# Kernel optimization log

Measured on AMD Instinct MI355X. Metric: run time of the kernel, lower is better.

The kernel has to match this reference:

```python
import jax, jax.numpy as jnp
import numpy as np

N, E = 50000, 800000
DIM_IN, DIM_H, DIM_OUT, HEADS = 128, 32, 16, 4
HID = DIM_H * HEADS  # 128
FINAL = DIM_OUT * HEADS  # 64
NEG_SLOPE = 0.2


def _glorot(key, shape):
    fan_in, fan_out = shape[0], shape[-1] if len(shape) > 1 else shape[0]
    lim = jnp.sqrt(6.0 / (fan_in + fan_out)).astype(jnp.float32)
    return jax.random.uniform(key, shape, jnp.float32, -lim, lim)


def setup_inputs() -> dict:
    key = jax.random.key(0)
    ks = jax.random.split(key, 16)
    x = jax.random.normal(ks[0], (N, DIM_IN), jnp.float32)
    edge_index = jax.random.randint(ks[1], (2, E), 0, N, dtype=jnp.int64)
    inp = {"x": x, "edge_index": edge_index}
    # layer 1: DIM_IN -> HEADS*DIM_H
    inp["Wl1"] = _glorot(ks[2], (DIM_IN, HEADS * DIM_H))
    inp["Wr1"] = _glorot(ks[3], (DIM_IN, HEADS * DIM_H))
    inp["att1"] = _glorot(ks[4], (HEADS, DIM_H))
    inp["b1"] = jnp.zeros((HEADS * DIM_H,), jnp.float32)
    # layer 2: HID -> HEADS*DIM_H
    inp["Wl2"] = _glorot(ks[5], (HID, HEADS * DIM_H))
    inp["Wr2"] = _glorot(ks[6], (HID, HEADS * DIM_H))
    inp["att2"] = _glorot(ks[7], (HEADS, DIM_H))
    inp["b2"] = jnp.zeros((HEADS * DIM_H,), jnp.float32)
    # layer 3: HID -> HEADS*DIM_OUT
    inp["Wl3"] = _glorot(ks[8], (HID, HEADS * DIM_OUT))
    inp["Wr3"] = _glorot(ks[9], (HID, HEADS * DIM_OUT))
    inp["att3"] = _glorot(ks[10], (HEADS, DIM_OUT))
    inp["b3"] = jnp.zeros((HEADS * DIM_OUT,), jnp.float32)
    return inp


def gatv2_conv(x, src, dst, Wl, Wr, att, b, heads, ch):
    n = x.shape[0]
    xl = (x @ Wl).reshape(n, heads, ch)  # source-side transform
    xr = (x @ Wr).reshape(n, heads, ch)  # target-side transform
    m = xl[src] + xr[dst]                 # [E, H, C]
    e = jnp.einsum('ehc,hc->eh', jax.nn.leaky_relu(m, NEG_SLOPE), att)
    # segment softmax over incoming edges of each dst node
    emax = jax.ops.segment_max(e, dst, num_segments=n)
    ex = jnp.exp(e - emax[dst])
    denom = jax.ops.segment_sum(ex, dst, num_segments=n)
    alpha = ex / denom[dst]               # [E, H]
    out = jax.ops.segment_sum(alpha[:, :, None] * xl[src], dst, num_segments=n)
    return out.reshape(n, heads * ch) + b


def reference(x, edge_index, Wl1, Wr1, att1, b1, Wl2, Wr2, att2, b2, Wl3, Wr3, att3, b3):
    n = x.shape[0]
    loops = jnp.arange(n, dtype=edge_index.dtype)
    src = jnp.concatenate([edge_index[0], loops])  # PyG add_self_loops=True
    dst = jnp.concatenate([edge_index[1], loops])
    # dropout is identity in eval mode
    h = jax.nn.elu(gatv2_conv(x, src, dst, Wl1, Wr1, att1, b1, HEADS, DIM_H))
    h = jax.nn.elu(gatv2_conv(h, src, dst, Wl2, Wr2, att2, b2, HEADS, DIM_H))
    h = gatv2_conv(h, src, dst, Wl3, Wr3, att3, b3, HEADS, DIM_OUT)
    return jax.nn.log_softmax(h, axis=1)
```

## Files before the change

kernel.cpp:

```cpp
#include <hip/hip_runtime.h>
#include <math.h>

constexpr int DIN  = 128;
constexpr int FSH  = 8;
constexpr int NFBM = 200;
constexpr int LCAP = 72;
constexpr int RND  = 4096;
constexpr int FCAP = 4608;

typedef __attribute__((ext_vector_type(8))) short short8;
typedef __attribute__((ext_vector_type(4))) float f32x4;

__device__ __forceinline__ unsigned short f2bf(float f) {
  unsigned u = __float_as_uint(f);
  u = (u + 0x7FFF + ((u >> 16) & 1)) >> 16;
  return (unsigned short)u;
}
__device__ __forceinline__ float bflo(unsigned u) { return __uint_as_float(u << 16); }
__device__ __forceinline__ float bfhi(unsigned u) { return __uint_as_float(u & 0xFFFF0000u); }

__device__ __forceinline__ void unpack8(uint4 u, float* x) {
  x[0] = bflo(u.x); x[1] = bfhi(u.x); x[2] = bflo(u.y); x[3] = bfhi(u.y);
  x[4] = bflo(u.z); x[5] = bfhi(u.z); x[6] = bflo(u.w); x[7] = bfhi(u.w);
}
__device__ __forceinline__ void unpack4(uint2 u, float* x) {
  x[0] = bflo(u.x); x[1] = bfhi(u.x); x[2] = bflo(u.y); x[3] = bfhi(u.y);
}

typedef const __attribute__((address_space(1))) unsigned int guint_t;
typedef __attribute__((address_space(3))) unsigned int luint_t;
__device__ __forceinline__ void async16(const void* g, void* l) {
  __builtin_amdgcn_global_load_lds((guint_t*)g, (luint_t*)l, 16, 0, 0);
}


__global__ __launch_bounds__(256) void prep_kernel(const int* __restrict__ ei,
    int* __restrict__ gcnt, unsigned* __restrict__ gpairs, int E, int nfb, int appb,
    const float* __restrict__ Wl1, const float* __restrict__ Wr1,
    const float* __restrict__ Wl2, const float* __restrict__ Wr2,
    const float* __restrict__ Wl3, const float* __restrict__ Wr3,
    unsigned short* __restrict__ Wt) {
  __shared__ unsigned buf[NFBM * LCAP];
  __shared__ int cnt[NFBM];
  __shared__ int gbase[NFBM];
  const int tid = threadIdx.x;

  if (blockIdx.x >= appb) {
    int e = (blockIdx.x - appb) * 256 + tid;
    if (e >= 81920) return;
    const float* src; int N; int off;
    if (e < 65536) {
      int m = e >> 14; off = e & 16383; N = 128;
      src = (m == 0) ? Wl1 : (m == 1) ? Wr1 : (m == 2) ? Wl2 : Wr2;
    } else {
      int e2 = e - 65536; int m = e2 >> 13; off = e2 & 8191; N = 64;
      src = m ? Wr3 : Wl3;
    }
    int nn = off >> 7, k = off & 127;
    Wt[e] = f2bf(src[(size_t)k * N + nn]);
    return;
  }

  if (tid < NFBM) cnt[tid] = 0;
  __syncthreads();

  const int k0 = blockIdx.x * RND;
  for (int i = tid; i < RND; i += 256) {
    int k = k0 + i;
    if (k >= E) break;
    int src = ei[k], dst = ei[E + k];
    int fb = dst >> FSH;
    int pos = atomicAdd(&cnt[fb], 1);
    if (pos < LCAP)
      buf[fb * LCAP + pos] = (unsigned)src | ((unsigned)(dst & ((1 << FSH) - 1)) << 16);
  }
  __syncthreads();

  if (tid < nfb) gbase[tid] = atomicAdd(&gcnt[tid], min(cnt[tid], LCAP));
  __syncthreads();

  const int wid = tid >> 6, lane = tid & 63;
  for (int fb = wid; fb < nfb; fb += 4) {
    int c  = min(cnt[fb], LCAP);
    int gb = gbase[fb];
    if (gb >= FCAP) continue;
    c = min(c, FCAP - gb);
    unsigned* dstp = gpairs + (size_t)fb * FCAP + gb;
    const unsigned* srcp = &buf[fb * LCAP];
    for (int i = lane; i < c; i += 64) dstp[i] = srcp[i];
  }
}


struct BuildSmem { int hist[1 << FSH]; int wsum[4]; int base_s; };

__device__ __forceinline__ void build_body(BuildSmem& s, int b,
    const unsigned* __restrict__ gpairs, const int* __restrict__ gcnt,
    int* __restrict__ row_ptr, unsigned short* __restrict__ edge_src,
    int n, int nfb) {
  const int tid = threadIdx.x;
  const int lane = tid & 63, wid = tid >> 6;

  const int d0 = b << FSH;
  const int nvalid = min(1 << FSH, n - d0);

  if (wid == 0) {
    int term = 0;
    for (int i = lane; i < b; i += 64)
      term += min(gcnt[i], FCAP) + min(1 << FSH, n - (i << FSH));
#pragma unroll
    for (int o = 32; o >= 1; o >>= 1) term += __shfl_xor(term, o, 64);
    if (lane == 0) s.base_s = term;
  }
  s.hist[tid] = (tid < nvalid) ? 1 : 0;
  __syncthreads();

  const int cnt = min(gcnt[b], FCAP);
  const unsigned* bp = gpairs + (size_t)b * FCAP;
  for (int i = tid; i < cnt; i += 256)
    atomicAdd(&s.hist[bp[i] >> 16], 1);
  __syncthreads();

  const int h = s.hist[tid];
  int incl = h;
#pragma unroll
  for (int o = 1; o < 64; o <<= 1) {
    int t = __shfl_up(incl, o, 64);
    if (lane >= o) incl += t;
  }
  if (lane == 63) s.wsum[wid] = incl;
  __syncthreads();
  int wo = 0;
  for (int wq = 0; wq < wid; ++wq) wo += s.wsum[wq];
  const int base = s.base_s;
  const int excl = wo + incl - h;
  if (tid < nvalid) {
    row_ptr[d0 + tid] = base + excl;
    edge_src[base + excl] = (unsigned short)(d0 + tid);
    s.hist[tid] = excl + 1;
  } else if (d0 + tid == n) {
    row_ptr[n] = base + excl;
  }
  if (b == nfb - 1 && d0 + (1 << FSH) <= n && tid == 0)
    row_ptr[n] = base + cnt + nvalid;
  __syncthreads();

  for (int i = tid; i < cnt; i += 256) {
    unsigned p = bp[i];
    int pos = atomicAdd(&s.hist[p >> 16], 1);
    edge_src[base + pos] = (unsigned short)(p & 0xFFFFu);
  }
}


template<int NC, bool CVT>
__device__ __forceinline__ void gemm2_body(char* lds, int bid, const void* __restrict__ Ap,
    const unsigned short* __restrict__ Wlt, const unsigned short* __restrict__ Wrt,
    unsigned short* __restrict__ outl, unsigned short* __restrict__ outr, int M) {
  constexpr int WNB = NC / 16;
  char* As = lds;
  char* Ws = lds + 16384;
  const int tid  = threadIdx.x;
  const int w    = tid >> 6, lane = tid & 63;
  const int q    = lane >> 4, r15 = lane & 15;
  const int row0 = bid * 64;

  if constexpr (CVT) {
    const float* Af = (const float*)Ap;
    for (int idx = tid * 4; idx < 64 * 128; idx += 1024) {
      int rl = idx >> 7, k = idx & 127;
      int rg = row0 + rl; if (rg >= M) rg = M - 1;
      float4 v = *(const float4*)&Af[(size_t)rg * 128 + k];
      uint2 pk;
      pk.x = (unsigned)f2bf(v.x) | ((unsigned)f2bf(v.y) << 16);
      pk.y = (unsigned)f2bf(v.z) | ((unsigned)f2bf(v.w) << 16);
      char* addr = As + (rl >> 4) * 4096 + (k >> 5) * 1024 +
                   ((((k >> 3) & 3) * 16) + (rl & 15)) * 16 + (k & 7) * 2;
      *(uint2*)addr = pk;
    }
  } else {
    const unsigned short* A = (const unsigned short*)Ap;
    int r = row0 + w * 16 + r15; if (r >= M) r = M - 1;
    const char* g = (const char*)A + (size_t)r * 256 + q * 16;
    char* l = As + w * 4096;
#pragma unroll
    for (int kk = 0; kk < 4; ++kk) async16(g + kk * 64, l + kk * 1024);
  }
  for (int nt = w; nt < WNB; nt += 4) {
    const char* g = (const char*)Wlt + ((size_t)(nt * 16 + r15)) * 256 + q * 16;
    char* l = Ws + nt * 4096;
#pragma unroll
    for (int kk = 0; kk < 4; ++kk) async16(g + kk * 64, l + kk * 1024);
  }
  __syncthreads();

  const char* aw = As + w * 4096;
  f32x4 acc[WNB] = {};
#pragma unroll
  for (int kk = 0; kk < 4; ++kk) {
    short8 af = *(const short8*)(aw + kk * 1024 + (size_t)lane * 16);
#pragma unroll
    for (int nt = 0; nt < WNB; ++nt) {
      short8 bf = *(const short8*)(Ws + (nt * 4 + kk) * 1024 + (size_t)lane * 16);
      acc[nt] = __builtin_amdgcn_mfma_f32_16x16x32_bf16(af, bf, acc[nt], 0, 0, 0);
    }
  }
  {
    int rowb = row0 + w * 16 + q * 4;
#pragma unroll
    for (int nt = 0; nt < WNB; ++nt)
#pragma unroll
      for (int r = 0; r < 4; ++r) {
        int rr = rowb + r;
        if (rr < M) outl[(size_t)rr * NC + nt * 16 + r15] = f2bf(acc[nt][r]);
      }
  }
  __syncthreads();
  for (int nt = w; nt < WNB; nt += 4) {
    const char* g = (const char*)Wrt + ((size_t)(nt * 16 + r15)) * 256 + q * 16;
    char* l = Ws + nt * 4096;
#pragma unroll
    for (int kk = 0; kk < 4; ++kk) async16(g + kk * 64, l + kk * 1024);
  }
  __syncthreads();

  f32x4 acc2[WNB] = {};
#pragma unroll
  for (int kk = 0; kk < 4; ++kk) {
    short8 af = *(const short8*)(aw + kk * 1024 + (size_t)lane * 16);
#pragma unroll
    for (int nt = 0; nt < WNB; ++nt) {
      short8 bf = *(const short8*)(Ws + (nt * 4 + kk) * 1024 + (size_t)lane * 16);
      acc2[nt] = __builtin_amdgcn_mfma_f32_16x16x32_bf16(af, bf, acc2[nt], 0, 0, 0);
    }
  }
  {
    int rowb = row0 + w * 16 + q * 4;
#pragma unroll
    for (int nt = 0; nt < WNB; ++nt)
#pragma unroll
      for (int r = 0; r < 4; ++r) {
        int rr = rowb + r;
        if (rr < M) outr[(size_t)rr * NC + nt * 16 + r15] = f2bf(acc2[nt][r]);
      }
  }
}


union GemmBuildSmem { char lds[16384 + 128 * 256]; BuildSmem b; };

__global__ __launch_bounds__(256) void gemm1_build_kernel(const void* __restrict__ Ap,
    const unsigned short* __restrict__ Wlt, const unsigned short* __restrict__ Wrt,
    unsigned short* __restrict__ outl, unsigned short* __restrict__ outr,
    const unsigned* __restrict__ gpairs, const int* __restrict__ gcnt,
    int* __restrict__ row_ptr, unsigned short* __restrict__ edge_src,
    int n, int nfb) {
  __shared__ GemmBuildSmem smem;
  if (blockIdx.x < (unsigned)nfb)
    build_body(smem.b, blockIdx.x, gpairs, gcnt, row_ptr, edge_src, n, nfb);
  else
    gemm2_body<128, true>(smem.lds, blockIdx.x - nfb, Ap, Wlt, Wrt, outl, outr, n);
}


__device__ __forceinline__ uint4 agg128_node(
    const unsigned short* __restrict__ xl, const unsigned short* xr,
    const float* __restrict__ att, const float* __restrict__ bias,
    const int* __restrict__ row_ptr, const unsigned short* __restrict__ edge_src,
    int node, int c0) {
  float xrv[8];
  unpack8(*(const uint4*)&xr[(size_t)node * 128 + c0], xrv);
  float a6[8], a4[8];
  {
    float4 aa = *(const float4*)&att[c0];
    float4 ab = *(const float4*)&att[c0 + 4];
    float at[8] = {aa.x, aa.y, aa.z, aa.w, ab.x, ab.y, ab.z, ab.w};
#pragma unroll
    for (int j = 0; j < 8; ++j) { a6[j] = 0.6f * at[j]; a4[j] = 0.4f * at[j]; }
  }

  float l = 0.f, o[8] = {};
  int idx = row_ptr[node];
  const int end = row_ptr[node + 1];

  int s0 = 0, s1 = 0, s2 = 0, s3 = 0;
  if (idx + 4 <= end) {
    s0 = edge_src[idx];     s1 = edge_src[idx + 1];
    s2 = edge_src[idx + 2]; s3 = edge_src[idx + 3];
  }
  while (idx + 4 <= end) {
    uint4 u0 = *(const uint4*)&xl[(size_t)s0 * 128 + c0];
    uint4 u1 = *(const uint4*)&xl[(size_t)s1 * 128 + c0];
    uint4 u2 = *(const uint4*)&xl[(size_t)s2 * 128 + c0];
    uint4 u3 = *(const uint4*)&xl[(size_t)s3 * 128 + c0];
    idx += 4;
    if (idx + 4 <= end) {
      s0 = edge_src[idx];     s1 = edge_src[idx + 1];
      s2 = edge_src[idx + 2]; s3 = edge_src[idx + 3];
    }
    float x0[8], x1[8], x2[8], x3[8];
    unpack8(u0, x0); unpack8(u1, x1); unpack8(u2, x2); unpack8(u3, x3);
    float p0 = 0.f, p1 = 0.f, p2 = 0.f, p3 = 0.f;
#pragma unroll
    for (int j = 0; j < 8; ++j) {
      float t0 = x0[j] + xrv[j], t1 = x1[j] + xrv[j];
      float t2 = x2[j] + xrv[j], t3 = x3[j] + xrv[j];
      p0 = fmaf(t0, a6[j], p0); p0 = fmaf(fabsf(t0), a4[j], p0);
      p1 = fmaf(t1, a6[j], p1); p1 = fmaf(fabsf(t1), a4[j], p1);
      p2 = fmaf(t2, a6[j], p2); p2 = fmaf(fabsf(t2), a4[j], p2);
      p3 = fmaf(t3, a6[j], p3); p3 = fmaf(fabsf(t3), a4[j], p3);
    }
    p0 += __shfl_xor(p0, 1, 64); p0 += __shfl_xor(p0, 2, 64);
    p1 += __shfl_xor(p1, 1, 64); p1 += __shfl_xor(p1, 2, 64);
    p2 += __shfl_xor(p2, 1, 64); p2 += __shfl_xor(p2, 2, 64);
    p3 += __shfl_xor(p3, 1, 64); p3 += __shfl_xor(p3, 2, 64);
    float e0 = __expf(fminf(p0, 80.f)), e1 = __expf(fminf(p1, 80.f));
    float e2 = __expf(fminf(p2, 80.f)), e3 = __expf(fminf(p3, 80.f));
    l += (e0 + e1) + (e2 + e3);
#pragma unroll
    for (int j = 0; j < 8; ++j)
      o[j] = fmaf(e0, x0[j], fmaf(e1, x1[j], fmaf(e2, x2[j], fmaf(e3, x3[j], o[j]))));
  }
  for (; idx < end; ++idx) {
    int s = edge_src[idx];
    uint4 u0 = *(const uint4*)&xl[(size_t)s * 128 + c0];
    float x0[8];
    unpack8(u0, x0);
    float p0 = 0.f;
#pragma unroll
    for (int j = 0; j < 8; ++j) {
      float t = x0[j] + xrv[j];
      p0 = fmaf(t, a6[j], p0); p0 = fmaf(fabsf(t), a4[j], p0);
    }
    p0 += __shfl_xor(p0, 1, 64); p0 += __shfl_xor(p0, 2, 64);
    float e0 = __expf(fminf(p0, 80.f));
    l += e0;
#pragma unroll
    for (int j = 0; j < 8; ++j) o[j] = fmaf(e0, x0[j], o[j]);
  }

  float4 b0 = *(const float4*)&bias[c0];
  float4 b1 = *(const float4*)&bias[c0 + 4];
  float bb[8] = {b0.x, b0.y, b0.z, b0.w, b1.x, b1.y, b1.z, b1.w};
  float rl = 1.f / l;
  unsigned short res[8];
#pragma unroll
  for (int j = 0; j < 8; ++j) {
    float v = o[j] * rl + bb[j];
    v = v > 0.f ? v : __expf(v) - 1.f;
    res[j] = f2bf(v);
  }
  uint4 ov;
  ov.x = (unsigned)res[0] | ((unsigned)res[1] << 16);
  ov.y = (unsigned)res[2] | ((unsigned)res[3] << 16);
  ov.z = (unsigned)res[4] | ((unsigned)res[5] << 16);
  ov.w = (unsigned)res[6] | ((unsigned)res[7] << 16);
  return ov;
}


template<int NC>
__global__ __launch_bounds__(512, 4) void agg_gemm_kernel(
    const unsigned short* __restrict__ xg,
    const unsigned short* xr,
    const float* __restrict__ att, const float* __restrict__ bias,
    const int* __restrict__ row_ptr, const unsigned short* __restrict__ edge_src,
    const unsigned short* __restrict__ Wlt, const unsigned short* __restrict__ Wrt,
    unsigned short* outl, unsigned short* outr, int n) {
  constexpr int WNB = NC / 16;
  __shared__ char lds[16384 + 2 * NC * 256];
  char* As  = lds;
  char* WsL = lds + 16384;
  char* WsR = WsL + NC * 256;
  const int tid  = threadIdx.x;
  const int w8   = tid >> 6, lane = tid & 63;
  const int q    = lane >> 4, r15 = lane & 15;
  const int row0 = blockIdx.x * 64;

  {
    const unsigned short* Wsrc = (w8 < 4) ? Wlt : Wrt;
    char* Wdst = (w8 < 4) ? WsL : WsR;
    const int wq = w8 & 3;
    for (int nt = wq; nt < WNB; nt += 4) {
      const char* g = (const char*)Wsrc + ((size_t)(nt * 16 + r15)) * 256 + q * 16;
      char* l = Wdst + nt * 4096;
#pragma unroll
      for (int kk = 0; kk < 4; ++kk) async16(g + kk * 64, l + kk * 1024);
    }
  }

  const int r   = tid & 15;
  const int g16 = tid >> 4;
  const int c0  = r * 8;
#pragma unroll
  for (int pass = 0; pass < 2; ++pass) {
    const int rl   = pass * 32 + g16;
    const int node = row0 + rl;
    uint4 ov = make_uint4(0, 0, 0, 0);
    if (node < n)
      ov = agg128_node(xg, xr, att, bias, row_ptr, edge_src, node, c0);
    char* addr = As + (rl >> 4) * 4096 + (r >> 2) * 1024 +
                 (((r & 3) * 16) + (rl & 15)) * 16;
    *(uint4*)addr = ov;
  }
  __syncthreads();

  const char* Wsme = (w8 < 4) ? WsL : WsR;
  unsigned short* outme = (w8 < 4) ? outl : outr;
  const int wq = w8 & 3;
  const char* aw = As + wq * 4096;
  f32x4 acc[WNB] = {};
#pragma unroll
  for (int kk = 0; kk < 4; ++kk) {
    short8 af = *(const short8*)(aw + kk * 1024 + (size_t)lane * 16);
#pragma unroll
    for (int nt = 0; nt < WNB; ++nt) {
      short8 bf = *(const short8*)(Wsme + (nt * 4 + kk) * 1024 + (size_t)lane * 16);
      acc[nt] = __builtin_amdgcn_mfma_f32_16x16x32_bf16(af, bf, acc[nt], 0, 0, 0);
    }
  }
  const int rowb = row0 + wq * 16 + q * 4;
#pragma unroll
  for (int nt = 0; nt < WNB; ++nt)
#pragma unroll
    for (int rr4 = 0; rr4 < 4; ++rr4) {
      int rr = rowb + rr4;
      if (rr < n) outme[(size_t)rr * NC + nt * 16 + r15] = f2bf(acc[nt][rr4]);
    }
}


__global__ __launch_bounds__(256) void aggregate64_kernel(
    const unsigned short* __restrict__ xl, const unsigned short* __restrict__ xr,
    const float* __restrict__ att, const float* __restrict__ bias,
    const int* __restrict__ row_ptr, const unsigned short* __restrict__ edge_src,
    float* __restrict__ out, int n) {
  const int tid  = threadIdx.x;
  const int r    = tid & 15;
  const int node = blockIdx.x * 16 + (tid >> 4);
  if (node >= n) return;
  const int c0 = r * 4;

  float xrv[4];
  unpack4(*(const uint2*)&xr[(size_t)node * 64 + c0], xrv);
  float a6[4], a4[4];
  {
    float4 aa = *(const float4*)&att[c0];
    float at[4] = {aa.x, aa.y, aa.z, aa.w};
#pragma unroll
    for (int j = 0; j < 4; ++j) { a6[j] = 0.6f * at[j]; a4[j] = 0.4f * at[j]; }
  }

  float l = 0.f, o[4] = {};
  int idx = row_ptr[node];
  const int end = row_ptr[node + 1];

  int s0 = 0, s1 = 0, s2 = 0, s3 = 0;
  if (idx + 4 <= end) {
    s0 = edge_src[idx];     s1 = edge_src[idx + 1];
    s2 = edge_src[idx + 2]; s3 = edge_src[idx + 3];
  }
  while (idx + 4 <= end) {
    uint2 u0 = *(const uint2*)&xl[(size_t)s0 * 64 + c0];
    uint2 u1 = *(const uint2*)&xl[(size_t)s1 * 64 + c0];
    uint2 u2 = *(const uint2*)&xl[(size_t)s2 * 64 + c0];
    uint2 u3 = *(const uint2*)&xl[(size_t)s3 * 64 + c0];
    idx += 4;
    if (idx + 4 <= end) {
      s0 = edge_src[idx];     s1 = edge_src[idx + 1];
      s2 = edge_src[idx + 2]; s3 = edge_src[idx + 3];
    }
    float x0[4], x1[4], x2[4], x3[4];
    unpack4(u0, x0); unpack4(u1, x1); unpack4(u2, x2); unpack4(u3, x3);
    float p0 = 0.f, p1 = 0.f, p2 = 0.f, p3 = 0.f;
#pragma unroll
    for (int j = 0; j < 4; ++j) {
      float t0 = x0[j] + xrv[j], t1 = x1[j] + xrv[j];
      float t2 = x2[j] + xrv[j], t3 = x3[j] + xrv[j];
      p0 = fmaf(t0, a6[j], p0); p0 = fmaf(fabsf(t0), a4[j], p0);
      p1 = fmaf(t1, a6[j], p1); p1 = fmaf(fabsf(t1), a4[j], p1);
      p2 = fmaf(t2, a6[j], p2); p2 = fmaf(fabsf(t2), a4[j], p2);
      p3 = fmaf(t3, a6[j], p3); p3 = fmaf(fabsf(t3), a4[j], p3);
    }
    p0 += __shfl_xor(p0, 1, 64); p0 += __shfl_xor(p0, 2, 64);
    p1 += __shfl_xor(p1, 1, 64); p1 += __shfl_xor(p1, 2, 64);
    p2 += __shfl_xor(p2, 1, 64); p2 += __shfl_xor(p2, 2, 64);
    p3 += __shfl_xor(p3, 1, 64); p3 += __shfl_xor(p3, 2, 64);
    float e0 = __expf(fminf(p0, 80.f)), e1 = __expf(fminf(p1, 80.f));
    float e2 = __expf(fminf(p2, 80.f)), e3 = __expf(fminf(p3, 80.f));
    l += (e0 + e1) + (e2 + e3);
#pragma unroll
    for (int j = 0; j < 4; ++j)
      o[j] = fmaf(e0, x0[j], fmaf(e1, x1[j], fmaf(e2, x2[j], fmaf(e3, x3[j], o[j]))));
  }
  for (; idx < end; ++idx) {
    int s = edge_src[idx];
    uint2 u0 = *(const uint2*)&xl[(size_t)s * 64 + c0];
    float x0[4];
    unpack4(u0, x0);
    float p0 = 0.f;
#pragma unroll
    for (int j = 0; j < 4; ++j) {
      float t = x0[j] + xrv[j];
      p0 = fmaf(t, a6[j], p0); p0 = fmaf(fabsf(t), a4[j], p0);
    }
    p0 += __shfl_xor(p0, 1, 64); p0 += __shfl_xor(p0, 2, 64);
    float e0 = __expf(fminf(p0, 80.f));
    l += e0;
#pragma unroll
    for (int j = 0; j < 4; ++j) o[j] = fmaf(e0, x0[j], o[j]);
  }

  float4 bv = *(const float4*)&bias[c0];
  float bb[4] = {bv.x, bv.y, bv.z, bv.w};
  float rl = 1.f / l;
  float rr[4];
#pragma unroll
  for (int j = 0; j < 4; ++j) rr[j] = o[j] * rl + bb[j];

  float mx = fmaxf(fmaxf(rr[0], rr[1]), fmaxf(rr[2], rr[3]));
#pragma unroll
  for (int off = 1; off < 16; off <<= 1) mx = fmaxf(mx, __shfl_xor(mx, off, 64));
  float se = __expf(rr[0] - mx) + __expf(rr[1] - mx) +
             __expf(rr[2] - mx) + __expf(rr[3] - mx);
#pragma unroll
  for (int off = 1; off < 16; off <<= 1) se += __shfl_xor(se, off, 64);
  float ls = mx + __logf(se);
  *(float4*)&out[(size_t)node * 64 + c0] =
      make_float4(rr[0] - ls, rr[1] - ls, rr[2] - ls, rr[3] - ls);
}


extern "C" void kernel_launch(void* const* d_in, const int* in_sizes, int n_in,
                              void* d_out, int out_size, void* d_ws, size_t ws_size,
                              hipStream_t stream) {
  const float* x    = (const float*)d_in[0];
  const int*   ei   = (const int*)d_in[1];
  const float* Wl1  = (const float*)d_in[2];
  const float* Wr1  = (const float*)d_in[3];
  const float* att1 = (const float*)d_in[4];
  const float* b1   = (const float*)d_in[5];
  const float* Wl2  = (const float*)d_in[6];
  const float* Wr2  = (const float*)d_in[7];
  const float* att2 = (const float*)d_in[8];
  const float* b2   = (const float*)d_in[9];
  const float* Wl3  = (const float*)d_in[10];
  const float* Wr3  = (const float*)d_in[11];
  const float* att3 = (const float*)d_in[12];
  const float* b3   = (const float*)d_in[13];
  const int n = in_sizes[0] / DIN;
  const int E = in_sizes[1] / 2;
  float* out = (float*)d_out;

  const int nfb  = (n + (1 << FSH) - 1) >> FSH;
  const int appb = (E + RND - 1) / RND;

  unsigned short* xl = (unsigned short*)d_ws;
  unsigned short* xr = xl + (size_t)n * 128;
  unsigned short* h  = xr + (size_t)n * 128;
  unsigned short* Wt = h + (size_t)n * 128;
  unsigned short* Wl1t = Wt, *Wr1t = Wt + 16384;
  unsigned short* Wl2t = Wt + 32768, *Wr2t = Wt + 49152;
  unsigned short* Wl3t = Wt + 65536, *Wr3t = Wt + 73728;
  int* row_ptr  = (int*)(Wt + 81920);
  int* gcnt     = row_ptr + (n + 16);
  unsigned short* edge_src = (unsigned short*)(gcnt + NFBM);
  unsigned* gpairs = (unsigned*)((char*)edge_src +
      ((((size_t)(E + n) * 2) + 15) & ~(size_t)15));

  hipMemsetAsync(gcnt, 0, NFBM * sizeof(int), stream);

  prep_kernel<<<appb + 320, 256, 0, stream>>>(ei, gcnt, gpairs, E, nfb, appb,
                                              Wl1, Wr1, Wl2, Wr2, Wl3, Wr3, Wt);

  const int gb = (n + 63) / 64;
  const int ab = (n + 15) / 16;

  gemm1_build_kernel<<<nfb + gb, 256, 0, stream>>>(x, Wl1t, Wr1t, xl, xr,
                                                   gpairs, gcnt, row_ptr, edge_src, n, nfb);

  agg_gemm_kernel<128><<<gb, 512, 0, stream>>>(xl, xr, att1, b1, row_ptr, edge_src,
                                               Wl2t, Wr2t, h, xr, n);

  agg_gemm_kernel<64><<<gb, 512, 0, stream>>>(h, xr, att2, b2, row_ptr, edge_src,
                                              Wl3t, Wr3t, xl, xl + (size_t)n * 64, n);

  aggregate64_kernel<<<ab, 256, 0, stream>>>(xl, xl + (size_t)n * 64, att3, b3,
                                             row_ptr, edge_src, out, n);
}
```

Baseline: 261.3 us.

## Halve LDS weight buffer in agg_gemm by staging Wl then Wr sequentially

The fused aggregate+GEMM kernel used to keep both Wl and Wr tiles in LDS at once, with half the waves computing each output. Now one weight buffer holds Wl first: all 8 waves split its column tiles and write outl. Then Wr is loaded into the same buffer and used for outr. This halves the weight LDS footprint and cuts the accumulator count per wave, and the launch bound is raised from 4 to 6 blocks to get more occupancy for the latency-bound gather. The cost is two extra barriers and a Wr load that is serialized after the first GEMM instead of overlapping with aggregation.

```diff
diff --git a/kernel.cpp b/kernel.cpp
--- a/kernel.cpp
+++ b/kernel.cpp
@@ -360,7 +360,7 @@
 
 
 template<int NC>
-__global__ __launch_bounds__(512, 4) void agg_gemm_kernel(
+__global__ __launch_bounds__(512, 6) void agg_gemm_kernel(
     const unsigned short* __restrict__ xg,
     const unsigned short* xr,
     const float* __restrict__ att, const float* __restrict__ bias,
@@ -368,25 +368,20 @@
     const unsigned short* __restrict__ Wlt, const unsigned short* __restrict__ Wrt,
     unsigned short* outl, unsigned short* outr, int n) {
   constexpr int WNB = NC / 16;
-  __shared__ char lds[16384 + 2 * NC * 256];
-  char* As  = lds;
-  char* WsL = lds + 16384;
-  char* WsR = WsL + NC * 256;
+  constexpr int NT2 = WNB / 2;
+  __shared__ char lds[16384 + NC * 256];
+  char* As = lds;
+  char* Ws = lds + 16384;
   const int tid  = threadIdx.x;
   const int w8   = tid >> 6, lane = tid & 63;
   const int q    = lane >> 4, r15 = lane & 15;
   const int row0 = blockIdx.x * 64;
 
-  {
-    const unsigned short* Wsrc = (w8 < 4) ? Wlt : Wrt;
-    char* Wdst = (w8 < 4) ? WsL : WsR;
-    const int wq = w8 & 3;
-    for (int nt = wq; nt < WNB; nt += 4) {
-      const char* g = (const char*)Wsrc + ((size_t)(nt * 16 + r15)) * 256 + q * 16;
-      char* l = Wdst + nt * 4096;
-#pragma unroll
-      for (int kk = 0; kk < 4; ++kk) async16(g + kk * 64, l + kk * 1024);
-    }
+  for (int nt = w8; nt < WNB; nt += 8) {
+    const char* g = (const char*)Wlt + ((size_t)(nt * 16 + r15)) * 256 + q * 16;
+    char* l = Ws + nt * 4096;
+#pragma unroll
+    for (int kk = 0; kk < 4; ++kk) async16(g + kk * 64, l + kk * 1024);
   }
 
   const int r   = tid & 15;
@@ -405,28 +400,59 @@
   }
   __syncthreads();
 
-  const char* Wsme = (w8 < 4) ? WsL : WsR;
-  unsigned short* outme = (w8 < 4) ? outl : outr;
   const int wq = w8 & 3;
+  const int nh = w8 >> 2;
   const char* aw = As + wq * 4096;
-  f32x4 acc[WNB] = {};
-#pragma unroll
-  for (int kk = 0; kk < 4; ++kk) {
-    short8 af = *(const short8*)(aw + kk * 1024 + (size_t)lane * 16);
-#pragma unroll
-    for (int nt = 0; nt < WNB; ++nt) {
-      short8 bf = *(const short8*)(Wsme + (nt * 4 + kk) * 1024 + (size_t)lane * 16);
-      acc[nt] = __builtin_amdgcn_mfma_f32_16x16x32_bf16(af, bf, acc[nt], 0, 0, 0);
-    }
-  }
   const int rowb = row0 + wq * 16 + q * 4;
-#pragma unroll
-  for (int nt = 0; nt < WNB; ++nt)
-#pragma unroll
-    for (int rr4 = 0; rr4 < 4; ++rr4) {
-      int rr = rowb + rr4;
-      if (rr < n) outme[(size_t)rr * NC + nt * 16 + r15] = f2bf(acc[nt][rr4]);
-    }
+
+  {
+    f32x4 acc[NT2] = {};
+#pragma unroll
+    for (int kk = 0; kk < 4; ++kk) {
+      short8 af = *(const short8*)(aw + kk * 1024 + (size_t)lane * 16);
+#pragma unroll
+      for (int t = 0; t < NT2; ++t) {
+        short8 bf = *(const short8*)(Ws + ((nh * NT2 + t) * 4 + kk) * 1024 + (size_t)lane * 16);
+        acc[t] = __builtin_amdgcn_mfma_f32_16x16x32_bf16(af, bf, acc[t], 0, 0, 0);
+      }
+    }
+#pragma unroll
+    for (int t = 0; t < NT2; ++t)
+#pragma unroll
+      for (int rr4 = 0; rr4 < 4; ++rr4) {
+        int rr = rowb + rr4;
+        if (rr < n) outl[(size_t)rr * NC + (nh * NT2 + t) * 16 + r15] = f2bf(acc[t][rr4]);
+      }
+  }
+  __syncthreads();
+
+  for (int nt = w8; nt < WNB; nt += 8) {
+    const char* g = (const char*)Wrt + ((size_t)(nt * 16 + r15)) * 256 + q * 16;
+    char* l = Ws + nt * 4096;
+#pragma unroll
+    for (int kk = 0; kk < 4; ++kk) async16(g + kk * 64, l + kk * 1024);
+  }
+  __syncthreads();
+
+  {
+    f32x4 acc[NT2] = {};
+#pragma unroll
+    for (int kk = 0; kk < 4; ++kk) {
+      short8 af = *(const short8*)(aw + kk * 1024 + (size_t)lane * 16);
+#pragma unroll
+      for (int t = 0; t < NT2; ++t) {
+        short8 bf = *(const short8*)(Ws + ((nh * NT2 + t) * 4 + kk) * 1024 + (size_t)lane * 16);
+        acc[t] = __builtin_amdgcn_mfma_f32_16x16x32_bf16(af, bf, acc[t], 0, 0, 0);
+      }
+    }
+#pragma unroll
+    for (int t = 0; t < NT2; ++t)
+#pragma unroll
+      for (int rr4 = 0; rr4 < 4; ++rr4) {
+        int rr = rowb + rr4;
+        if (rr < n) outr[(size_t)rr * NC + (nh * NT2 + t) * 16 + r15] = f2bf(acc[t][rr4]);
+      }
+  }
 }
 
 
```

Result: slower. 334.3 us (+27.9%).
